# Optimization experiments

Measured on AMD Instinct MI355X. Metric: run time of the kernel, lower is better.

The kernel has to match this reference:

```python
import jax, jax.numpy as jnp
import numpy as np

N = 50000       # num nodes
E = 800000      # num edges (before self loops)
D_IN = 128
D_H = 128
D_OUT = 40


def setup_inputs() -> dict:
    key = jax.random.key(0)
    ks = jax.random.split(key, 8)
    x = jax.random.normal(ks[0], (N, D_IN), dtype=jnp.float32)
    edge_index = jax.random.randint(ks[1], (2, E), 0, N, dtype=jnp.int32)
    # GCNConv weights (glorot-ish scale) and biases
    W1 = jax.random.normal(ks[2], (D_IN, D_H), dtype=jnp.float32) / np.sqrt(D_IN)
    b1 = jnp.zeros((D_H,), dtype=jnp.float32)
    W2 = jax.random.normal(ks[3], (D_H, D_H), dtype=jnp.float32) / np.sqrt(D_H)
    b2 = jnp.zeros((D_H,), dtype=jnp.float32)
    Wc = jax.random.normal(ks[4], (D_H, D_OUT), dtype=jnp.float32) / np.sqrt(D_H)
    bc = jnp.zeros((D_OUT,), dtype=jnp.float32)
    return {"x": x, "edge_index": edge_index, "W1": W1, "b1": b1,
            "W2": W2, "b2": b2, "Wc": Wc, "bc": bc}


def _gcn_conv(x, row, col, num_nodes, W, b):
    # PyG GCNConv: h = X @ W; out[c] += norm(r,c) * h[r]; out += b
    h = x @ W
    deg = jax.ops.segment_sum(jnp.ones(row.shape[0], h.dtype), col,
                              num_segments=num_nodes)
    dinv = jnp.where(deg > 0, jax.lax.rsqrt(deg), 0.0).astype(h.dtype)
    norm = dinv[row] * dinv[col]                      # [E+N]
    msg = h[row] * norm[:, None]                      # gather + scale
    agg = jax.ops.segment_sum(msg, col, num_segments=num_nodes)  # scatter-add
    return agg + b


def reference(x, edge_index, W1, b1, W2, b2, Wc, bc):
    # add self loops (GCNConv default add_self_loops=True)
    loops = jnp.arange(N, dtype=edge_index.dtype)
    row = jnp.concatenate([edge_index[0], loops])
    col = jnp.concatenate([edge_index[1], loops])
    h = jax.nn.relu(_gcn_conv(x, row, col, N, W1, b1))
    h = jax.nn.relu(_gcn_conv(h, row, col, N, W2, b2))
    g = jnp.mean(h, axis=0)                           # mean pool over nodes
    return g @ Wc + bc                                # [D_OUT]
```

## Files before the change

kernel.cpp:

```cpp
#include <hip/hip_runtime.h>
#include <hip/hip_fp16.h>


constexpr int N = 50000;
constexpr int E = 800000;
constexpr int D = 128;
constexpr int DOUT = 40;
constexpr int CAP = 64;
constexpr int HB = 256;
constexpr int EPB = (E + HB - 1) / HB;
constexpr int HW = 12500;
constexpr int GM = (N + 127) / 128;
constexpr int NW = N / 4;
constexpr int GF = 5 * 131;

__global__ __launch_bounds__(256) void k_hist(const int* __restrict__ col,
                                              unsigned char* __restrict__ hist) {
    __shared__ unsigned int h[HW];
    int b = blockIdx.x, t = threadIdx.x;
    for (int i = t; i < HW; i += 256) h[i] = 0;
    __syncthreads();
    int e0 = b * EPB, e1 = e0 + EPB;
    if (e1 > E) e1 = E;
    for (int e = e0 + t; e < e1; e += 256) {
        int c = col[e];
        atomicAdd(&h[c >> 2], 1u << ((c & 3) * 8));
    }
    __syncthreads();
    unsigned int* out = (unsigned int*)(hist + (size_t)b * 50000);
    for (int i = t; i < HW; i += 256) out[i] = h[i];
}

__global__ void k_colscan(unsigned char* __restrict__ hist, int* __restrict__ deg) {
    int c = blockIdx.x * 256 + threadIdx.x;
    if (c >= N) return;
    int sum = 0;
    for (int b = 0; b < HB; ++b) {
        size_t idx = (size_t)b * 50000 + c;
        int v = hist[idx];
        hist[idx] = (unsigned char)sum;
        sum += v;
    }
    deg[c] = sum;
}

__device__ __forceinline__ float4 ld4(const float* p) { return *(const float4*)p; }
__device__ __forceinline__ float4 ld4(const __half* p) {
    uint2 u = *(const uint2*)p;
    __half2* h = (__half2*)&u;
    float2 a = __half22float2(h[0]), b = __half22float2(h[1]);
    return make_float4(a.x, a.y, b.x, b.y);
}

template <typename TA>
__device__ __forceinline__ void gemm128(const TA* __restrict__ A,
                                        const float* __restrict__ W,
                                        __half* __restrict__ outH,
                                        int row0, int tid,
                                        float (*As)[132], float (*Bs)[132]) {
    int tx = tid & 15, ty = tid >> 4;
    float acc[8][8] = {};

    for (int kt = 0; kt < 128; kt += 32) {
        {
            int r = tid >> 1;
            int kk = (tid & 1) * 16;
            int grow = row0 + r;
#pragma unroll
            for (int q = 0; q < 4; ++q) {
                float4 v = make_float4(0.f, 0.f, 0.f, 0.f);
                if (grow < N) v = ld4(&A[(size_t)grow * D + kt + kk + q * 4]);
                As[kk + q * 4 + 0][r] = v.x;
                As[kk + q * 4 + 1][r] = v.y;
                As[kk + q * 4 + 2][r] = v.z;
                As[kk + q * 4 + 3][r] = v.w;
            }
        }
        {
            int kb = tid >> 3;
            int cb = (tid & 7) * 16;
#pragma unroll
            for (int q = 0; q < 4; ++q) {
                *(float4*)&Bs[kb][cb + q * 4] =
                    *(const float4*)&W[(size_t)(kt + kb) * D + cb + q * 4];
            }
        }
        __syncthreads();
#pragma unroll
        for (int k = 0; k < 32; ++k) {
            float a[8], bb[8];
            *(float4*)&a[0] = *(const float4*)&As[k][ty * 8];
            *(float4*)&a[4] = *(const float4*)&As[k][ty * 8 + 4];
            *(float4*)&bb[0] = *(const float4*)&Bs[k][tx * 4];
            *(float4*)&bb[4] = *(const float4*)&Bs[k][64 + tx * 4];
#pragma unroll
            for (int i = 0; i < 8; ++i)
#pragma unroll
                for (int j = 0; j < 8; ++j)
                    acc[i][j] = fmaf(a[i], bb[j], acc[i][j]);
        }
        __syncthreads();
    }

#pragma unroll
    for (int i = 0; i < 8; ++i) {
        int r = row0 + ty * 8 + i;
        if (r < N) {
            union { __half2 h[2]; uint2 u; } p0, p1;
            p0.h[0] = __floats2half2_rn(acc[i][0], acc[i][1]);
            p0.h[1] = __floats2half2_rn(acc[i][2], acc[i][3]);
            p1.h[0] = __floats2half2_rn(acc[i][4], acc[i][5]);
            p1.h[1] = __floats2half2_rn(acc[i][6], acc[i][7]);
            *(uint2*)&outH[(size_t)r * D + tx * 4]      = p0.u;
            *(uint2*)&outH[(size_t)r * D + 64 + tx * 4] = p1.u;
        }
    }
}

__global__ __launch_bounds__(256) void k_fuse(const int* __restrict__ ei,
                                              const unsigned char* __restrict__ hist,
                                              unsigned short* __restrict__ csr,
                                              const float* __restrict__ A,
                                              const float* __restrict__ W,
                                              __half* __restrict__ outH) {
    __shared__ __align__(16) unsigned char smem[50048];
    int b = blockIdx.x, m = b % 5;

    if (m < 2) {
        int sb = (b / 5) * 2 + m;
        if (sb >= HB) return;
        unsigned int* h = (unsigned int*)smem;
        int t = threadIdx.x;
        for (int i = t; i < HW; i += 256) h[i] = 0;
        __syncthreads();
        const unsigned char* pref = hist + (size_t)sb * 50000;
        int e0 = sb * EPB, e1 = e0 + EPB;
        if (e1 > E) e1 = E;
        for (int e = e0 + t; e < e1; e += 256) {
            int c = ei[E + e];
            int r = ei[e];
            unsigned int old = atomicAdd(&h[c >> 2], 1u << ((c & 3) * 8));
            int rank = (old >> ((c & 3) * 8)) & 0xff;
            int slot = (int)pref[c] + rank;
            if (slot < CAP) csr[(c << 6) + slot] = (unsigned short)r;
        }
        return;
    }
    int gb = (b / 5) * 3 + (m - 2);
    if (gb >= GM) return;
    float (*As)[132] = (float (*)[132])smem;
    float (*Bs)[132] = (float (*)[132])(smem + 32 * 132 * 4);
    gemm128<float>(A, W, outH, gb * 128, threadIdx.x, As, Bs);
}

__global__ __launch_bounds__(256) void k_gemm(const __half* __restrict__ A,
                                              const float* __restrict__ W,
                                              __half* __restrict__ outH) {
    __shared__ float As[32][132];
    __shared__ float Bs[32][132];
    gemm128<__half>(A, W, outH, blockIdx.x * 128, threadIdx.x, As, Bs);
}

__device__ __forceinline__ void acc8(float* a, float w, uint4 u) {
    __half2* hp = (__half2*)&u;
#pragma unroll
    for (int i = 0; i < 4; ++i) {
        float2 f = __half22float2(hp[i]);
        a[2 * i]     = fmaf(w, f.x, a[2 * i]);
        a[2 * i + 1] = fmaf(w, f.y, a[2 * i + 1]);
    }
}

__device__ __forceinline__ float agg_core(int c, int lane,
                                          const __half* __restrict__ hsH,
                                          const int* __restrict__ deg,
                                          const unsigned short* __restrict__ csr,
                                          float* a0) {
    int qw = lane >> 4;
    int q  = lane & 15;
    int dgRaw = deg[c];
    int dg = dgRaw < CAP ? dgRaw : CAP;
    float dc = rsqrtf((float)(dgRaw + 1));
    int e0 = c << 6;

    float a1[8] = {0, 0, 0, 0, 0, 0, 0, 0};
#pragma unroll
    for (int t = 0; t < 8; ++t) a0[t] = 0.f;
    if (qw == 0) {
        uint4 u = *(const uint4*)&hsH[(size_t)c * D + q * 8];
        acc8(a0, dc, u);
    }

    int j = 0;
    for (; j + 8 <= dg; j += 8) {
        int r0 = csr[e0 + j + qw];
        int r1 = csr[e0 + j + 4 + qw];
        float w0 = rsqrtf((float)(deg[r0] + 1));
        float w1 = rsqrtf((float)(deg[r1] + 1));
        uint4 u0 = *(const uint4*)&hsH[(size_t)r0 * D + q * 8];
        uint4 u1 = *(const uint4*)&hsH[(size_t)r1 * D + q * 8];
        acc8(a0, w0, u0);
        acc8(a1, w1, u1);
    }
    if (j + 4 <= dg) {
        int r0 = csr[e0 + j + qw];
        float w0 = rsqrtf((float)(deg[r0] + 1));
        uint4 u0 = *(const uint4*)&hsH[(size_t)r0 * D + q * 8];
        acc8(a0, w0, u0);
        j += 4;
    }
    int rem = dg - j;
    if (qw < rem) {
        int r0 = csr[e0 + j + qw];
        float w0 = rsqrtf((float)(deg[r0] + 1));
        uint4 u0 = *(const uint4*)&hsH[(size_t)r0 * D + q * 8];
        acc8(a0, w0, u0);
    }

#pragma unroll
    for (int t = 0; t < 8; ++t) a0[t] += a1[t];
#pragma unroll
    for (int t = 0; t < 8; ++t) a0[t] += __shfl_xor(a0[t], 16, 64);
#pragma unroll
    for (int t = 0; t < 8; ++t) a0[t] += __shfl_xor(a0[t], 32, 64);
    return dc;
}

__global__ __launch_bounds__(256) void k_agg1(const __half* __restrict__ hsH,
                                              const int* __restrict__ deg,
                                              const unsigned short* __restrict__ csr,
                                              const float* __restrict__ bias,
                                              __half* __restrict__ outH) {
    int wave = threadIdx.x >> 6;
    int lane = threadIdx.x & 63;
    int c = blockIdx.x * 4 + wave;
    float a0[8];
    float dc = agg_core(c, lane, hsH, deg, csr, a0);
    if ((lane >> 4) == 0) {
        int q = lane & 15;
        union { __half2 h[4]; uint4 u; } p;
#pragma unroll
        for (int i = 0; i < 4; ++i) {
            float x = fmaxf(fmaf(dc, a0[2 * i],     bias[q * 8 + 2 * i]),     0.f);
            float y = fmaxf(fmaf(dc, a0[2 * i + 1], bias[q * 8 + 2 * i + 1]), 0.f);
            p.h[i] = __floats2half2_rn(x, y);
        }
        *(uint4*)&outH[(size_t)c * D + q * 8] = p.u;
    }
}

__global__ __launch_bounds__(256) void k_agg2(const __half* __restrict__ hsH,
                                              const int* __restrict__ deg,
                                              const unsigned short* __restrict__ csr,
                                              const float* __restrict__ bias,
                                              float* __restrict__ gpart) {
    __shared__ float gblk[4][128];
    int wave = threadIdx.x >> 6;
    int lane = threadIdx.x & 63;
    int c = blockIdx.x * 4 + wave;
    float a0[8];
    float dc = agg_core(c, lane, hsH, deg, csr, a0);
    if ((lane >> 4) == 0) {
        int q = lane & 15;
#pragma unroll
        for (int i = 0; i < 8; ++i)
            gblk[wave][q * 8 + i] = fmaxf(fmaf(dc, a0[i], bias[q * 8 + i]), 0.f);
    }
    __syncthreads();
    int t = threadIdx.x;
    if (t < 128)
        gpart[(size_t)blockIdx.x * 128 + t] =
            gblk[0][t] + gblk[1][t] + gblk[2][t] + gblk[3][t];
}

__global__ __launch_bounds__(256) void k_pool(const float* __restrict__ gpart,
                                              float* __restrict__ gpart2) {
    int d = threadIdx.x & 127;
    int half = threadIdx.x >> 7;
    int b = blockIdx.x;
    int per = (NW + 255) / 256;
    int r0 = b * per;
    int r1 = r0 + per;
    if (r1 > NW) r1 = NW;
    float acc = 0.f;
    for (int r = r0 + half; r < r1; r += 2)
        acc += gpart[(size_t)r * D + d];
    __shared__ float red[256];
    red[threadIdx.x] = acc;
    __syncthreads();
    if (half == 0) gpart2[(size_t)b * D + d] = red[d] + red[128 + d];
}

__global__ __launch_bounds__(512) void k_final(const float* __restrict__ gpart2,
                                               const float* __restrict__ Wc,
                                               const float* __restrict__ bc,
                                               float* __restrict__ out) {
    __shared__ float g[D];
    __shared__ float red[512];
    int t = threadIdx.x;
    int d = t & 127, grp = t >> 7;
    float s = 0.f;
#pragma unroll 4
    for (int w = grp * 64; w < grp * 64 + 64; ++w)
        s += gpart2[(size_t)w * D + d];
    red[t] = s;
    __syncthreads();
    if (grp == 0)
        g[d] = (red[d] + red[128 + d] + red[256 + d] + red[384 + d]) * (1.0f / (float)N);
    __syncthreads();
    if (t < DOUT) {
        float acc = bc[t];
        for (int dd = 0; dd < D; ++dd) acc = fmaf(g[dd], Wc[dd * DOUT + t], acc);
        out[t] = acc;
    }
}

extern "C" void kernel_launch(void* const* d_in, const int* in_sizes, int n_in,
                              void* d_out, int out_size, void* d_ws, size_t ws_size,
                              hipStream_t stream) {
    const float* x  = (const float*)d_in[0];
    const int*   ei = (const int*)d_in[1];
    const float* W1 = (const float*)d_in[2];
    const float* b1 = (const float*)d_in[3];
    const float* W2 = (const float*)d_in[4];
    const float* b2 = (const float*)d_in[5];
    const float* Wc = (const float*)d_in[6];
    const float* bc = (const float*)d_in[7];
    float* out = (float*)d_out;

    char* ws = (char*)d_ws;
    size_t off = 0;
    auto alloc = [&](size_t bytes) {
        void* p = ws + off;
        off += (bytes + 511) & ~(size_t)511;
        return p;
    };
    unsigned char*  hist   = (unsigned char*) alloc((size_t)HB * 50000);
    int*            deg    = (int*)           alloc((size_t)N * 4);
    unsigned short* csr    = (unsigned short*)alloc((size_t)N * CAP * 2);
    __half*         hsH    = (__half*)        alloc((size_t)N * D * 2);
    __half*         hactH  = (__half*)        alloc((size_t)N * D * 2);
    float*          gpart  = (float*)         alloc((size_t)NW * D * 4);
    float*          gpart2 = (float*)         alloc((size_t)256 * D * 4);
    (void)ws_size; (void)in_sizes; (void)n_in; (void)out_size;

    const int* col = ei + E;

    k_hist<<<HB, 256, 0, stream>>>(col, hist);
    k_colscan<<<(N + 255) / 256, 256, 0, stream>>>(hist, deg);
    k_fuse<<<GF, 256, 0, stream>>>(ei, hist, csr, x, W1, hsH);

    k_agg1<<<NW, 256, 0, stream>>>(hsH, deg, csr, b1, hactH);
    k_gemm<<<GM, 256, 0, stream>>>(hactH, W2, hsH);
    k_agg2<<<NW, 256, 0, stream>>>(hsH, deg, csr, b2, gpart);
    k_pool<<<256, 256, 0, stream>>>(gpart, gpart2);
    k_final<<<1, 512, 0, stream>>>(gpart2, Wc, bc, out);
}
```

Baseline: 254.5 us.

## Prescale GEMM output rows by dinv to drop per-edge degree lookups

```diff
diff --git a/kernel.cpp b/kernel.cpp
--- a/kernel.cpp
+++ b/kernel.cpp
@@ -31,10 +31,12 @@
     for (int i = t; i < HW; i += 256) out[i] = h[i];
 }
 
-__global__ void k_colscan(unsigned char* __restrict__ hist, int* __restrict__ deg) {
+__global__ void k_colscan(unsigned char* __restrict__ hist, int* __restrict__ deg,
+                          float* __restrict__ dinv) {
     int c = blockIdx.x * 256 + threadIdx.x;
     if (c >= N) return;
     int sum = 0;
+#pragma unroll 8
     for (int b = 0; b < HB; ++b) {
         size_t idx = (size_t)b * 50000 + c;
         int v = hist[idx];
@@ -42,6 +44,7 @@
         sum += v;
     }
     deg[c] = sum;
+    dinv[c] = rsqrtf((float)(sum + 1));
 }
 
 __device__ __forceinline__ float4 ld4(const float* p) { return *(const float4*)p; }
@@ -55,6 +58,7 @@
 template <typename TA>
 __device__ __forceinline__ void gemm128(const TA* __restrict__ A,
                                         const float* __restrict__ W,
+                                        const float* __restrict__ dinv,
                                         __half* __restrict__ outH,
                                         int row0, int tid,
                                         float (*As)[132], float (*Bs)[132]) {
@@ -106,11 +110,12 @@
     for (int i = 0; i < 8; ++i) {
         int r = row0 + ty * 8 + i;
         if (r < N) {
+            float s = dinv[r];
             union { __half2 h[2]; uint2 u; } p0, p1;
-            p0.h[0] = __floats2half2_rn(acc[i][0], acc[i][1]);
-            p0.h[1] = __floats2half2_rn(acc[i][2], acc[i][3]);
-            p1.h[0] = __floats2half2_rn(acc[i][4], acc[i][5]);
-            p1.h[1] = __floats2half2_rn(acc[i][6], acc[i][7]);
+            p0.h[0] = __floats2half2_rn(acc[i][0] * s, acc[i][1] * s);
+            p0.h[1] = __floats2half2_rn(acc[i][2] * s, acc[i][3] * s);
+            p1.h[0] = __floats2half2_rn(acc[i][4] * s, acc[i][5] * s);
+            p1.h[1] = __floats2half2_rn(acc[i][6] * s, acc[i][7] * s);
             *(uint2*)&outH[(size_t)r * D + tx * 4]      = p0.u;
             *(uint2*)&outH[(size_t)r * D + 64 + tx * 4] = p1.u;
         }
@@ -122,6 +127,7 @@
                                               unsigned short* __restrict__ csr,
                                               const float* __restrict__ A,
                                               const float* __restrict__ W,
+                                              const float* __restrict__ dinv,
                                               __half* __restrict__ outH) {
     __shared__ __align__(16) unsigned char smem[50048];
     int b = blockIdx.x, m = b % 5;
@@ -130,18 +136,17 @@
         int sb = (b / 5) * 2 + m;
         if (sb >= HB) return;
         unsigned int* h = (unsigned int*)smem;
+        const unsigned int* prefw = (const unsigned int*)(hist + (size_t)sb * 50000);
         int t = threadIdx.x;
-        for (int i = t; i < HW; i += 256) h[i] = 0;
+        for (int i = t; i < HW; i += 256) h[i] = prefw[i];
         __syncthreads();
-        const unsigned char* pref = hist + (size_t)sb * 50000;
         int e0 = sb * EPB, e1 = e0 + EPB;
         if (e1 > E) e1 = E;
         for (int e = e0 + t; e < e1; e += 256) {
             int c = ei[E + e];
             int r = ei[e];
             unsigned int old = atomicAdd(&h[c >> 2], 1u << ((c & 3) * 8));
-            int rank = (old >> ((c & 3) * 8)) & 0xff;
-            int slot = (int)pref[c] + rank;
+            int slot = (old >> ((c & 3) * 8)) & 0xff;
             if (slot < CAP) csr[(c << 6) + slot] = (unsigned short)r;
         }
         return;
@@ -150,24 +155,25 @@
     if (gb >= GM) return;
     float (*As)[132] = (float (*)[132])smem;
     float (*Bs)[132] = (float (*)[132])(smem + 32 * 132 * 4);
-    gemm128<float>(A, W, outH, gb * 128, threadIdx.x, As, Bs);
+    gemm128<float>(A, W, dinv, outH, gb * 128, threadIdx.x, As, Bs);
 }
 
 __global__ __launch_bounds__(256) void k_gemm(const __half* __restrict__ A,
                                               const float* __restrict__ W,
+                                              const float* __restrict__ dinv,
                                               __half* __restrict__ outH) {
     __shared__ float As[32][132];
     __shared__ float Bs[32][132];
-    gemm128<__half>(A, W, outH, blockIdx.x * 128, threadIdx.x, As, Bs);
-}
-
-__device__ __forceinline__ void acc8(float* a, float w, uint4 u) {
+    gemm128<__half>(A, W, dinv, outH, blockIdx.x * 128, threadIdx.x, As, Bs);
+}
+
+__device__ __forceinline__ void add8(float* a, uint4 u) {
     __half2* hp = (__half2*)&u;
 #pragma unroll
     for (int i = 0; i < 4; ++i) {
         float2 f = __half22float2(hp[i]);
-        a[2 * i]     = fmaf(w, f.x, a[2 * i]);
-        a[2 * i + 1] = fmaf(w, f.y, a[2 * i + 1]);
+        a[2 * i]     += f.x;
+        a[2 * i + 1] += f.y;
     }
 }
 
@@ -186,35 +192,27 @@
     float a1[8] = {0, 0, 0, 0, 0, 0, 0, 0};
 #pragma unroll
     for (int t = 0; t < 8; ++t) a0[t] = 0.f;
-    if (qw == 0) {
-        uint4 u = *(const uint4*)&hsH[(size_t)c * D + q * 8];
-        acc8(a0, dc, u);
-    }
+    if (qw == 0)
+        add8(a0, *(const uint4*)&hsH[(size_t)c * D + q * 8]);
 
     int j = 0;
     for (; j + 8 <= dg; j += 8) {
         int r0 = csr[e0 + j + qw];
         int r1 = csr[e0 + j + 4 + qw];
-        float w0 = rsqrtf((float)(deg[r0] + 1));
-        float w1 = rsqrtf((float)(deg[r1] + 1));
         uint4 u0 = *(const uint4*)&hsH[(size_t)r0 * D + q * 8];
         uint4 u1 = *(const uint4*)&hsH[(size_t)r1 * D + q * 8];
-        acc8(a0, w0, u0);
-        acc8(a1, w1, u1);
+        add8(a0, u0);
+        add8(a1, u1);
     }
     if (j + 4 <= dg) {
         int r0 = csr[e0 + j + qw];
-        float w0 = rsqrtf((float)(deg[r0] + 1));
-        uint4 u0 = *(const uint4*)&hsH[(size_t)r0 * D + q * 8];
-        acc8(a0, w0, u0);
+        add8(a0, *(const uint4*)&hsH[(size_t)r0 * D + q * 8]);
         j += 4;
     }
     int rem = dg - j;
     if (qw < rem) {
         int r0 = csr[e0 + j + qw];
-        float w0 = rsqrtf((float)(deg[r0] + 1));
-        uint4 u0 = *(const uint4*)&hsH[(size_t)r0 * D + q * 8];
-        acc8(a0, w0, u0);
+        add8(a0, *(const uint4*)&hsH[(size_t)r0 * D + q * 8]);
     }
 
 #pragma unroll
@@ -337,6 +335,7 @@
     };
     unsigned char*  hist   = (unsigned char*) alloc((size_t)HB * 50000);
     int*            deg    = (int*)           alloc((size_t)N * 4);
+    float*          dinv   = (float*)         alloc((size_t)N * 4);
     unsigned short* csr    = (unsigned short*)alloc((size_t)N * CAP * 2);
     __half*         hsH    = (__half*)        alloc((size_t)N * D * 2);
     __half*         hactH  = (__half*)        alloc((size_t)N * D * 2);
@@ -347,11 +346,11 @@
     const int* col = ei + E;
 
     k_hist<<<HB, 256, 0, stream>>>(col, hist);
-    k_colscan<<<(N + 255) / 256, 256, 0, stream>>>(hist, deg);
-    k_fuse<<<GF, 256, 0, stream>>>(ei, hist, csr, x, W1, hsH);
+    k_colscan<<<(N + 255) / 256, 256, 0, stream>>>(hist, deg, dinv);
+    k_fuse<<<GF, 256, 0, stream>>>(ei, hist, csr, x, W1, dinv, hsH);
 
     k_agg1<<<NW, 256, 0, stream>>>(hsH, deg, csr, b1, hactH);
-    k_gemm<<<GM, 256, 0, stream>>>(hactH, W2, hsH);
+    k_gemm<<<GM, 256, 0, stream>>>(hactH, W2, dinv, hsH);
     k_agg2<<<NW, 256, 0, stream>>>(hsH, deg, csr, b2, gpart);
     k_pool<<<256, 256, 0, stream>>>(gpart, gpart2);
     k_final<<<1, 512, 0, stream>>>(gpart2, Wc, bc, out);
```

New measurement: 256.2 us. About the same (+0.7%).
